# Kernel tuning notes

Measured on AMD Instinct MI355X. Metric: run time of the kernel, lower is better.

Reference implementation:

```python
import jax, jax.numpy as jnp
import numpy as np

N = 20000        # nodes
NHID = 128       # hidden channels per head
HEADS = 4
E = 320000       # edges (before self-loops)
NLAYERS = 4
NCLASS = 40
DT, ALPHA, GAMMA = 1.0, 1.0, 1.0
NEG_SLOPE = 0.2  # PyG GATConv default


def setup_inputs() -> dict:
    key = jax.random.key(0)
    ks = jax.random.split(key, 8)
    s = 1.0 / np.sqrt(NHID)
    x = jax.random.normal(ks[0], (N, NHID), jnp.float32)
    src = jax.random.randint(ks[1], (E,), 0, N, dtype=jnp.int32)
    dst = jax.random.randint(ks[2], (E,), 0, N, dtype=jnp.int32)
    W = jax.random.normal(ks[3], (NHID, HEADS * NHID), jnp.float32) * s
    att_src = jax.random.normal(ks[4], (HEADS, NHID), jnp.float32) * s
    att_dst = jax.random.normal(ks[5], (HEADS, NHID), jnp.float32) * s
    bias = jnp.zeros((HEADS * NHID,), jnp.float32)
    Wr = jax.random.normal(ks[6], (NCLASS, NHID), jnp.float32) * s
    br = jnp.zeros((NCLASS,), jnp.float32)
    return {"x": x, "src": src, "dst": dst, "W": W, "att_src": att_src,
            "att_dst": att_dst, "bias": bias, "Wr": Wr, "br": br}


def reference(x, src, dst, W, att_src, att_dst, bias, Wr, br):
    # add self loops (PyG GATConv default)
    loop = jnp.arange(N, dtype=src.dtype)
    s_idx = jnp.concatenate([src, loop])
    d_idx = jnp.concatenate([dst, loop])

    def gat(X):
        # X: [N, NHID] -> out: [N, HEADS*NHID] (head-major, as PyG concat)
        h = (X @ W).reshape(N, HEADS, NHID)                  # [N,H,C]
        a_s = jnp.einsum('nhc,hc->nh', h, att_src)            # [N,H]
        a_d = jnp.einsum('nhc,hc->nh', h, att_dst)            # [N,H]
        e = jax.nn.leaky_relu(a_s[s_idx] + a_d[d_idx], NEG_SLOPE)  # [Etot,H]
        m = jax.ops.segment_max(e, d_idx, num_segments=N)     # scatter-softmax
        ex = jnp.exp(e - m[d_idx])
        den = jax.ops.segment_sum(ex, d_idx, num_segments=N)
        alpha = ex / den[d_idx]                               # [Etot,H]
        msg = h[s_idx] * alpha[..., None]                     # [Etot,H,C]
        out = jax.ops.segment_sum(msg, d_idx, num_segments=N)  # [N,H,C]
        return out.reshape(N, HEADS * NHID) + bias

    def step(carry, _):
        X, Y = carry
        # view(N, -1, nheads).mean(-1) on head-major [N, H*C] layout
        agg = jax.nn.elu(gat(X)).reshape(N, NHID, HEADS).mean(axis=-1)
        Y2 = Y + DT * (agg - ALPHA * Y - GAMMA * X)
        X2 = X + DT * Y2
        return (X2, Y2), (X2, Y2)

    (Xf, Yf), (Xs, Ys) = jax.lax.scan(step, (x, x), None, length=NLAYERS)
    X_all = jnp.concatenate([x[:, None], jnp.moveaxis(Xs, 0, 1)], axis=1)  # [N,L+1,C]
    Y_all = jnp.concatenate([x[:, None], jnp.moveaxis(Ys, 0, 1)], axis=1)
    out = Xf @ Wr.T + br                                     # [N, NCLASS]
    return out, X_all, Y_all
```

## Files before the change

kernel.cpp:

```cpp
#include <hip/hip_runtime.h>

typedef unsigned short u16;
typedef unsigned int u32;

#define N_NODES 20000
#define NE 320000
#define NLAYERS 4
#define NCLASS 40
#define NEG_SLOPE 0.2f
#define LSTRIDE ((NLAYERS + 1) * 128)

typedef __bf16 bf16x8 __attribute__((ext_vector_type(8)));
typedef float f32x4 __attribute__((ext_vector_type(4)));

__device__ inline u16 f2bf(float f) {
    u32 u = __float_as_uint(f);
    return (u16)((u + 0x7fffu + ((u >> 16) & 1u)) >> 16);
}
__device__ inline float bf2f(u16 u) { return __uint_as_float(((u32)u) << 16); }

__global__ void k_init(const float* __restrict__ x, u16* __restrict__ Xbf,
                       float* __restrict__ Xall, float* __restrict__ Yall) {
    int t = blockIdx.x * 256 + threadIdx.x;
    if (t >= N_NODES * 128) return;
    float v = x[t];
    Xbf[t] = f2bf(v);
    int n = t >> 7, c = t & 127;
    int ob = n * LSTRIDE + c;
    Xall[ob] = v;
    Yall[ob] = v;
}

__global__ void k_trans(const float* __restrict__ W, u16* __restrict__ Wt) {
    int t = blockIdx.x * 256 + threadIdx.x;
    int k = t >> 9, col = t & 511;
    Wt[col * 128 + k] = f2bf(W[t]);
}

__global__ __launch_bounds__(256) void k_fold(const float* __restrict__ W,
                                              const float* __restrict__ att_s,
                                              const float* __restrict__ att_d,
                                              float* __restrict__ Vs, float* __restrict__ Vd) {
    int wid = (blockIdx.x * 256 + threadIdx.x) >> 6;
    int lane = threadIdx.x & 63;
    int t = wid >> 2, hd = wid & 3;
    float w0 = W[t * 512 + hd * 128 + lane];
    float w1 = W[t * 512 + hd * 128 + 64 + lane];
    float s1 = w0 * att_s[hd * 128 + lane] + w1 * att_s[hd * 128 + 64 + lane];
    float s2 = w0 * att_d[hd * 128 + lane] + w1 * att_d[hd * 128 + 64 + lane];
    for (int off = 32; off; off >>= 1) {
        s1 += __shfl_xor(s1, off);
        s2 += __shfl_xor(s2, off);
    }
    if (lane == 0) {
        Vs[t * 4 + hd] = s1;
        Vd[t * 4 + hd] = s2;
    }
}

__global__ void k_ones(int* __restrict__ counts) {
    int t = blockIdx.x * 256 + threadIdx.x;
    if (t < N_NODES) counts[t] = 1;
}
__global__ void k_count(const int* __restrict__ dst, int* __restrict__ counts) {
    int t = blockIdx.x * 256 + threadIdx.x;
    if (t < NE) atomicAdd(&counts[dst[t]], 1);
}
__global__ void k_scan(const int* __restrict__ counts, int* __restrict__ indptr,
                       int* __restrict__ cursor) {
    __shared__ int part[1024];
    int t = threadIdx.x;
    const int CH = 20;
    int c0 = t * CH;
    int s = 0;
    for (int i = 0; i < CH; i++) {
        int idx = c0 + i;
        if (idx < N_NODES) s += counts[idx];
    }
    part[t] = s;
    __syncthreads();
    for (int off = 1; off < 1024; off <<= 1) {
        int v = 0;
        if (t >= off) v = part[t - off];
        __syncthreads();
        if (t >= off) part[t] += v;
        __syncthreads();
    }
    int ex = (t == 0) ? 0 : part[t - 1];
    for (int i = 0; i < CH; i++) {
        int idx = c0 + i;
        if (idx < N_NODES) {
            indptr[idx] = ex;
            cursor[idx] = ex;
            ex += counts[idx];
        }
    }
    if (t == 1023) indptr[N_NODES] = part[1023];
}
__global__ void k_scatter(const int* __restrict__ src, const int* __restrict__ dst,
                          int* __restrict__ cursor, int* __restrict__ esrc) {
    int t = blockIdx.x * 256 + threadIdx.x;
    if (t >= NE + N_NODES) return;
    int s, d;
    if (t < NE) { s = src[t]; d = dst[t]; }
    else { s = d = t - NE; }
    int pos = atomicAdd(&cursor[d], 1);
    esrc[pos] = s;
}

__global__ __launch_bounds__(256) void k_gemm(const u16* __restrict__ Xbf,
                                              const u16* __restrict__ Wt,
                                              u16* __restrict__ hbf) {
    const int r0 = blockIdx.x * 64;
    const int c0 = blockIdx.y * 64;
    __shared__ u16 As[64 * 136];
    __shared__ u16 Bs[64 * 136];
    const int t = threadIdx.x;
    for (int i = 0; i < 4; i++) {
        int flat = i * 256 + t;
        int row = flat >> 4;
        int kc = flat & 15;
        uint4 av = make_uint4(0u, 0u, 0u, 0u);
        int gr = r0 + row;
        if (gr < N_NODES) av = *(const uint4*)(Xbf + gr * 128 + kc * 8);
        *(uint4*)(As + row * 136 + kc * 8) = av;
        uint4 bv = *(const uint4*)(Wt + (c0 + row) * 128 + kc * 8);
        *(uint4*)(Bs + row * 136 + kc * 8) = bv;
    }
    __syncthreads();
    const int wave = t >> 6, lane = t & 63;
    const int wr = (wave >> 1) * 32, wc = (wave & 1) * 32;
    const int lrow = lane & 15, quad = lane >> 4;
    f32x4 acc[2][2] = {};
    for (int kk = 0; kk < 128; kk += 32) {
        bf16x8 a[2], b[2];
        for (int mi = 0; mi < 2; mi++)
            a[mi] = *(const bf16x8*)(As + (wr + mi * 16 + lrow) * 136 + kk + quad * 8);
        for (int ni = 0; ni < 2; ni++)
            b[ni] = *(const bf16x8*)(Bs + (wc + ni * 16 + lrow) * 136 + kk + quad * 8);
        for (int mi = 0; mi < 2; mi++)
            for (int ni = 0; ni < 2; ni++)
                acc[mi][ni] = __builtin_amdgcn_mfma_f32_16x16x32_bf16(a[mi], b[ni], acc[mi][ni], 0, 0, 0);
    }
    for (int mi = 0; mi < 2; mi++)
        for (int ni = 0; ni < 2; ni++)
            for (int r = 0; r < 4; r++) {
                int row = r0 + wr + mi * 16 + quad * 4 + r;
                int col = c0 + wc + ni * 16 + lrow;
                if (row < N_NODES) hbf[row * 512 + col] = f2bf(acc[mi][ni][r]);
            }
}

__global__ __launch_bounds__(256) void k_att(const float* __restrict__ Xall, int layer,
                                             const float* __restrict__ Vs,
                                             const float* __restrict__ Vd,
                                             float* __restrict__ a_s, float* __restrict__ a_d) {
    int wid = (blockIdx.x * 256 + threadIdx.x) >> 6;
    int lane = threadIdx.x & 63;
    const float* Xr = Xall + wid * LSTRIDE + layer * 128;
    float x0 = Xr[lane], x1 = Xr[64 + lane];
    f32x4 vs0 = *(const f32x4*)(Vs + lane * 4), vs1 = *(const f32x4*)(Vs + (64 + lane) * 4);
    f32x4 vd0 = *(const f32x4*)(Vd + lane * 4), vd1 = *(const f32x4*)(Vd + (64 + lane) * 4);
    f32x4 ps = x0 * vs0 + x1 * vs1;
    f32x4 pd = x0 * vd0 + x1 * vd1;
    for (int off = 32; off; off >>= 1)
        for (int c = 0; c < 4; c++) {
            ps[c] += __shfl_xor(ps[c], off);
            pd[c] += __shfl_xor(pd[c], off);
        }
    if (lane == 0) {
        *(f32x4*)(a_s + wid * 4) = ps;
        *(f32x4*)(a_d + wid * 4) = pd;
    }
}

__global__ __launch_bounds__(256) void k_aggr(
    const int* __restrict__ indptr, const int* __restrict__ esrc,
    const float* __restrict__ a_s, const float* __restrict__ a_d,
    const u16* __restrict__ hbf, const float* __restrict__ bias,
    u16* __restrict__ Xbf, float* __restrict__ Xall, float* __restrict__ Yall,
    float* __restrict__ a_s_nxt, float* __restrict__ a_d_nxt,
    const float* __restrict__ Vs, const float* __restrict__ Vd, int layer) {
    __shared__ int s_sh[4][66];
    __shared__ alignas(16) float al_sh[4][66][4];
    int d = (blockIdx.x * 256 + threadIdx.x) >> 6;
    int lane = threadIdx.x & 63;
    int w = threadIdx.x >> 6;
    int start = indptr[d], end = indptr[d + 1];
    int deg = end - start;
    f32x4 ad = *(const f32x4*)(a_d + d * 4);
    int hd = lane >> 4;
    float acc[8] = {0.f, 0.f, 0.f, 0.f, 0.f, 0.f, 0.f, 0.f};

    auto chunk_aggr = [&](int cnt) {
        int s_cur = s_sh[w][0];
        float al_cur = al_sh[w][0][hd];
        uint4 hv = *(const uint4*)(hbf + s_cur * 512 + lane * 8);
        for (int i = 0; i < cnt; i++) {
            int s_nxt = s_sh[w][i + 1];
            float al_nxt = al_sh[w][i + 1][hd];
            uint4 hv_n = *(const uint4*)(hbf + s_nxt * 512 + lane * 8);
            u32 h0 = hv.x, h1 = hv.y, h2 = hv.z, h3 = hv.w;
            acc[0] += al_cur * __uint_as_float(h0 << 16);
            acc[1] += al_cur * __uint_as_float(h0 & 0xffff0000u);
            acc[2] += al_cur * __uint_as_float(h1 << 16);
            acc[3] += al_cur * __uint_as_float(h1 & 0xffff0000u);
            acc[4] += al_cur * __uint_as_float(h2 << 16);
            acc[5] += al_cur * __uint_as_float(h2 & 0xffff0000u);
            acc[6] += al_cur * __uint_as_float(h3 << 16);
            acc[7] += al_cur * __uint_as_float(h3 & 0xffff0000u);
            hv = hv_n;
            al_cur = al_nxt;
        }
    };

    if (deg <= 64) {
        int j = start + lane;
        int s = 0;
        f32x4 e = {-1e30f, -1e30f, -1e30f, -1e30f};
        if (j < end) {
            s = esrc[j];
            f32x4 as = *(const f32x4*)(a_s + s * 4);
            for (int c = 0; c < 4; c++) {
                float v = as[c] + ad[c];
                e[c] = v > 0.f ? v : NEG_SLOPE * v;
            }
        }
        f32x4 mx = e;
        for (int off = 32; off; off >>= 1)
            for (int c = 0; c < 4; c++) mx[c] = fmaxf(mx[c], __shfl_xor(mx[c], off));
        f32x4 p;
        for (int c = 0; c < 4; c++) p[c] = __expf(e[c] - mx[c]);
        f32x4 den = p;
        for (int off = 32; off; off >>= 1)
            for (int c = 0; c < 4; c++) den[c] += __shfl_xor(den[c], off);
        f32x4 alpha;
        for (int c = 0; c < 4; c++) alpha[c] = p[c] * (1.f / den[c]);
        s_sh[w][lane] = s;
        *(f32x4*)&al_sh[w][lane][0] = alpha;
        if (lane == 63) {
            s_sh[w][64] = 0;
            f32x4 z = {0.f, 0.f, 0.f, 0.f};
            *(f32x4*)&al_sh[w][64][0] = z;
        }
        __builtin_amdgcn_wave_barrier();
        chunk_aggr(deg);
    } else {
        f32x4 mx = {-1e30f, -1e30f, -1e30f, -1e30f};
        for (int j = start + lane; j < end; j += 64) {
            int s = esrc[j];
            f32x4 e = *(const f32x4*)(a_s + s * 4) + ad;
            for (int c = 0; c < 4; c++) {
                float v = e[c];
                v = v > 0.f ? v : NEG_SLOPE * v;
                mx[c] = fmaxf(mx[c], v);
            }
        }
        for (int off = 32; off; off >>= 1)
            for (int c = 0; c < 4; c++) mx[c] = fmaxf(mx[c], __shfl_xor(mx[c], off));
        f32x4 den = {0.f, 0.f, 0.f, 0.f};
        for (int j = start + lane; j < end; j += 64) {
            int s = esrc[j];
            f32x4 e = *(const f32x4*)(a_s + s * 4) + ad;
            for (int c = 0; c < 4; c++) {
                float v = e[c];
                v = v > 0.f ? v : NEG_SLOPE * v;
                den[c] += __expf(v - mx[c]);
            }
        }
        for (int off = 32; off; off >>= 1)
            for (int c = 0; c < 4; c++) den[c] += __shfl_xor(den[c], off);
        f32x4 rd;
        for (int c = 0; c < 4; c++) rd[c] = 1.f / den[c];
        for (int base = start; base < end; base += 64) {
            int cnt = min(64, end - base);
            int jj = base + lane;
            int s = 0;
            f32x4 alpha = {0.f, 0.f, 0.f, 0.f};
            if (jj < end) {
                s = esrc[jj];
                f32x4 e = *(const f32x4*)(a_s + s * 4) + ad;
                for (int c = 0; c < 4; c++) {
                    float v = e[c];
                    v = v > 0.f ? v : NEG_SLOPE * v;
                    alpha[c] = __expf(v - mx[c]) * rd[c];
                }
            }
            s_sh[w][lane] = s;
            *(f32x4*)&al_sh[w][lane][0] = alpha;
            if (lane == 63) {
                s_sh[w][64] = 0;
                f32x4 z = {0.f, 0.f, 0.f, 0.f};
                *(f32x4*)&al_sh[w][64][0] = z;
            }
            __builtin_amdgcn_wave_barrier();
            chunk_aggr(cnt);
            __builtin_amdgcn_wave_barrier();
        }
    }

    f32x4 b0 = *(const f32x4*)(bias + lane * 8);
    f32x4 b1 = *(const f32x4*)(bias + lane * 8 + 4);
    float g[8];
    for (int i = 0; i < 4; i++) g[i] = acc[i] + b0[i];
    for (int i = 0; i < 4; i++) g[4 + i] = acc[4 + i] + b1[i];
    for (int i = 0; i < 8; i++) {
        float v = g[i];
        g[i] = v > 0.f ? v : __expf(v) - 1.f;
    }
    float agg0 = (g[0] + g[1] + g[2] + g[3]) * 0.25f;
    float agg1 = (g[4] + g[5] + g[6] + g[7]) * 0.25f;
    int i0 = lane * 2;
    int xo = d * LSTRIDE + layer * 128 + i0;
    int no = d * LSTRIDE + (layer + 1) * 128 + i0;
    float x0 = Xall[xo], x1 = Xall[xo + 1];
    Xall[no] = agg0;
    Xall[no + 1] = agg1;
    Yall[no] = agg0 - x0;
    Yall[no + 1] = agg1 - x1;
    Xbf[d * 128 + i0] = f2bf(agg0);
    Xbf[d * 128 + i0 + 1] = f2bf(agg1);

    f32x4 vs0 = *(const f32x4*)(Vs + i0 * 4), vs1 = *(const f32x4*)(Vs + (i0 + 1) * 4);
    f32x4 vd0 = *(const f32x4*)(Vd + i0 * 4), vd1 = *(const f32x4*)(Vd + (i0 + 1) * 4);
    f32x4 ps, pd;
    for (int c = 0; c < 4; c++) {
        ps[c] = agg0 * vs0[c] + agg1 * vs1[c];
        pd[c] = agg0 * vd0[c] + agg1 * vd1[c];
    }
    for (int off = 32; off; off >>= 1)
        for (int c = 0; c < 4; c++) {
            ps[c] += __shfl_xor(ps[c], off);
            pd[c] += __shfl_xor(pd[c], off);
        }
    if (lane == 0) {
        *(f32x4*)(a_s_nxt + d * 4) = ps;
        *(f32x4*)(a_d_nxt + d * 4) = pd;
    }
}

__global__ __launch_bounds__(256) void k_out(const float* __restrict__ Xall,
                                             const float* __restrict__ Wr,
                                             const float* __restrict__ br,
                                             float* __restrict__ out) {
    __shared__ float Xs[4][128];
    int wave = threadIdx.x >> 6, lane = threadIdx.x & 63;
    int n = blockIdx.x * 4 + wave;
    const float* Xr = Xall + n * LSTRIDE + NLAYERS * 128;
    Xs[wave][lane] = Xr[lane];
    Xs[wave][64 + lane] = Xr[64 + lane];
    __syncthreads();
    if (lane < NCLASS) {
        float acc = 0.f;
        for (int kc = 0; kc < 32; kc++) {
            f32x4 wv = *(const f32x4*)(Wr + lane * 128 + kc * 4);
            for (int q = 0; q < 4; q++) acc += Xs[wave][kc * 4 + q] * wv[q];
        }
        out[n * NCLASS + lane] = acc + br[lane];
    }
}

extern "C" void kernel_launch(void* const* d_in, const int* in_sizes, int n_in,
                              void* d_out, int out_size, void* d_ws, size_t ws_size,
                              hipStream_t stream) {
    const float* x = (const float*)d_in[0];
    const int* src = (const int*)d_in[1];
    const int* dst = (const int*)d_in[2];
    const float* W = (const float*)d_in[3];
    const float* att_s = (const float*)d_in[4];
    const float* att_d = (const float*)d_in[5];
    const float* bias = (const float*)d_in[6];
    const float* Wr = (const float*)d_in[7];
    const float* br = (const float*)d_in[8];

    float* out = (float*)d_out;
    float* Xall = out + (size_t)N_NODES * NCLASS;
    float* Yall = Xall + (size_t)N_NODES * LSTRIDE;

    char* p = (char*)d_ws;
    auto alloc = [&](size_t bytes) -> char* {
        char* r = p;
        p += (bytes + 255) & ~(size_t)255;
        return r;
    };
    u16* Xbf = (u16*)alloc((size_t)N_NODES * 128 * 2);
    u16* hbf = (u16*)alloc((size_t)N_NODES * 512 * 2);
    u16* Wt = (u16*)alloc(512 * 128 * 2);
    float* a_sA = (float*)alloc((size_t)N_NODES * 4 * 4);
    float* a_dA = (float*)alloc((size_t)N_NODES * 4 * 4);
    float* a_sB = (float*)alloc((size_t)N_NODES * 4 * 4);
    float* a_dB = (float*)alloc((size_t)N_NODES * 4 * 4);
    float* Vs = (float*)alloc(128 * 4 * 4);
    float* Vd = (float*)alloc(128 * 4 * 4);
    int* indptr = (int*)alloc((N_NODES + 1) * 4);
    int* cursor = (int*)alloc(N_NODES * 4);
    int* counts = (int*)alloc(N_NODES * 4);
    int* esrc = (int*)alloc((size_t)(NE + N_NODES) * 4);

    k_init<<<(N_NODES * 128 + 255) / 256, 256, 0, stream>>>(x, Xbf, Xall, Yall);
    k_trans<<<(512 * 128) / 256, 256, 0, stream>>>(W, Wt);
    k_fold<<<128, 256, 0, stream>>>(W, att_s, att_d, Vs, Vd);
    k_ones<<<(N_NODES + 255) / 256, 256, 0, stream>>>(counts);
    k_count<<<(NE + 255) / 256, 256, 0, stream>>>(dst, counts);
    k_scan<<<1, 1024, 0, stream>>>(counts, indptr, cursor);
    k_scatter<<<(NE + N_NODES + 255) / 256, 256, 0, stream>>>(src, dst, cursor, esrc);

    k_att<<<N_NODES / 4, 256, 0, stream>>>(Xall, 0, Vs, Vd, a_sA, a_dA);

    for (int layer = 0; layer < NLAYERS; layer++) {
        const float* as_r = (layer & 1) ? a_sB : a_sA;
        const float* ad_r = (layer & 1) ? a_dB : a_dA;
        float* as_w = (layer & 1) ? a_sA : a_sB;
        float* ad_w = (layer & 1) ? a_dA : a_dB;
        k_gemm<<<dim3((N_NODES + 63) / 64, 8), 256, 0, stream>>>(Xbf, Wt, hbf);
        k_aggr<<<N_NODES / 4, 256, 0, stream>>>(indptr, esrc, as_r, ad_r, hbf, bias,
                                                Xbf, Xall, Yall, as_w, ad_w, Vs, Vd, layer);
    }
    k_out<<<N_NODES / 4, 256, 0, stream>>>(Xall, Wr, br, out);
}
```

Before: 531.3 us.

## Aggregate raw node features before projection, then apply W per head after

Uses linearity to reorder aggregate-then-project. Each layer now gathers 128-wide bf16 X rows per edge, weighted by the four head attention coefficients, instead of gathering 512-wide projected h rows. A new fused kernel multiplies the per-head aggregates by W and applies bias, ELU, head mean, state update and next-layer logits. This cuts per-edge gather traffic about fourfold and replaces the separate GEMM. The cost is a staged N×512 intermediate buffer and an extra bf16 rounding of the aggregates. It also folds the counts initialisation into k_init and skips logits on the last layer.

Measured after the change: 500.8 us. -5.8%, faster.

```diff
diff --git a/kernel.cpp b/kernel.cpp
--- a/kernel.cpp
+++ b/kernel.cpp
@@ -20,9 +20,11 @@
 __device__ inline float bf2f(u16 u) { return __uint_as_float(((u32)u) << 16); }
 
 __global__ void k_init(const float* __restrict__ x, u16* __restrict__ Xbf,
-                       float* __restrict__ Xall, float* __restrict__ Yall) {
+                       float* __restrict__ Xall, float* __restrict__ Yall,
+                       int* __restrict__ counts) {
     int t = blockIdx.x * 256 + threadIdx.x;
     if (t >= N_NODES * 128) return;
+    if (t < N_NODES) counts[t] = 1;
     float v = x[t];
     Xbf[t] = f2bf(v);
     int n = t >> 7, c = t & 127;
@@ -58,10 +60,6 @@
     }
 }
 
-__global__ void k_ones(int* __restrict__ counts) {
-    int t = blockIdx.x * 256 + threadIdx.x;
-    if (t < N_NODES) counts[t] = 1;
-}
 __global__ void k_count(const int* __restrict__ dst, int* __restrict__ counts) {
     int t = blockIdx.x * 256 + threadIdx.x;
     if (t < NE) atomicAdd(&counts[dst[t]], 1);
@@ -106,49 +104,6 @@
     else { s = d = t - NE; }
     int pos = atomicAdd(&cursor[d], 1);
     esrc[pos] = s;
-}
-
-__global__ __launch_bounds__(256) void k_gemm(const u16* __restrict__ Xbf,
-                                              const u16* __restrict__ Wt,
-                                              u16* __restrict__ hbf) {
-    const int r0 = blockIdx.x * 64;
-    const int c0 = blockIdx.y * 64;
-    __shared__ u16 As[64 * 136];
-    __shared__ u16 Bs[64 * 136];
-    const int t = threadIdx.x;
-    for (int i = 0; i < 4; i++) {
-        int flat = i * 256 + t;
-        int row = flat >> 4;
-        int kc = flat & 15;
-        uint4 av = make_uint4(0u, 0u, 0u, 0u);
-        int gr = r0 + row;
-        if (gr < N_NODES) av = *(const uint4*)(Xbf + gr * 128 + kc * 8);
-        *(uint4*)(As + row * 136 + kc * 8) = av;
-        uint4 bv = *(const uint4*)(Wt + (c0 + row) * 128 + kc * 8);
-        *(uint4*)(Bs + row * 136 + kc * 8) = bv;
-    }
-    __syncthreads();
-    const int wave = t >> 6, lane = t & 63;
-    const int wr = (wave >> 1) * 32, wc = (wave & 1) * 32;
-    const int lrow = lane & 15, quad = lane >> 4;
-    f32x4 acc[2][2] = {};
-    for (int kk = 0; kk < 128; kk += 32) {
-        bf16x8 a[2], b[2];
-        for (int mi = 0; mi < 2; mi++)
-            a[mi] = *(const bf16x8*)(As + (wr + mi * 16 + lrow) * 136 + kk + quad * 8);
-        for (int ni = 0; ni < 2; ni++)
-            b[ni] = *(const bf16x8*)(Bs + (wc + ni * 16 + lrow) * 136 + kk + quad * 8);
-        for (int mi = 0; mi < 2; mi++)
-            for (int ni = 0; ni < 2; ni++)
-                acc[mi][ni] = __builtin_amdgcn_mfma_f32_16x16x32_bf16(a[mi], b[ni], acc[mi][ni], 0, 0, 0);
-    }
-    for (int mi = 0; mi < 2; mi++)
-        for (int ni = 0; ni < 2; ni++)
-            for (int r = 0; r < 4; r++) {
-                int row = r0 + wr + mi * 16 + quad * 4 + r;
-                int col = c0 + wc + ni * 16 + lrow;
-                if (row < N_NODES) hbf[row * 512 + col] = f2bf(acc[mi][ni][r]);
-            }
 }
 
 __global__ __launch_bounds__(256) void k_att(const float* __restrict__ Xall, int layer,
@@ -177,10 +132,7 @@
 __global__ __launch_bounds__(256) void k_aggr(
     const int* __restrict__ indptr, const int* __restrict__ esrc,
     const float* __restrict__ a_s, const float* __restrict__ a_d,
-    const u16* __restrict__ hbf, const float* __restrict__ bias,
-    u16* __restrict__ Xbf, float* __restrict__ Xall, float* __restrict__ Yall,
-    float* __restrict__ a_s_nxt, float* __restrict__ a_d_nxt,
-    const float* __restrict__ Vs, const float* __restrict__ Vd, int layer) {
+    const u16* __restrict__ Xbf, u16* __restrict__ Xagg) {
     __shared__ int s_sh[4][66];
     __shared__ alignas(16) float al_sh[4][66][4];
     int d = (blockIdx.x * 256 + threadIdx.x) >> 6;
@@ -189,27 +141,22 @@
     int start = indptr[d], end = indptr[d + 1];
     int deg = end - start;
     f32x4 ad = *(const f32x4*)(a_d + d * 4);
-    int hd = lane >> 4;
-    float acc[8] = {0.f, 0.f, 0.f, 0.f, 0.f, 0.f, 0.f, 0.f};
+    f32x4 accA = {0.f, 0.f, 0.f, 0.f};
+    f32x4 accB = {0.f, 0.f, 0.f, 0.f};
 
     auto chunk_aggr = [&](int cnt) {
         int s_cur = s_sh[w][0];
-        float al_cur = al_sh[w][0][hd];
-        uint4 hv = *(const uint4*)(hbf + s_cur * 512 + lane * 8);
+        f32x4 al_cur = *(const f32x4*)&al_sh[w][0][0];
+        u32 xv = *(const u32*)(Xbf + s_cur * 128 + lane * 2);
         for (int i = 0; i < cnt; i++) {
             int s_nxt = s_sh[w][i + 1];
-            float al_nxt = al_sh[w][i + 1][hd];
-            uint4 hv_n = *(const uint4*)(hbf + s_nxt * 512 + lane * 8);
-            u32 h0 = hv.x, h1 = hv.y, h2 = hv.z, h3 = hv.w;
-            acc[0] += al_cur * __uint_as_float(h0 << 16);
-            acc[1] += al_cur * __uint_as_float(h0 & 0xffff0000u);
-            acc[2] += al_cur * __uint_as_float(h1 << 16);
-            acc[3] += al_cur * __uint_as_float(h1 & 0xffff0000u);
-            acc[4] += al_cur * __uint_as_float(h2 << 16);
-            acc[5] += al_cur * __uint_as_float(h2 & 0xffff0000u);
-            acc[6] += al_cur * __uint_as_float(h3 << 16);
-            acc[7] += al_cur * __uint_as_float(h3 & 0xffff0000u);
-            hv = hv_n;
+            f32x4 al_nxt = *(const f32x4*)&al_sh[w][i + 1][0];
+            u32 xv_n = *(const u32*)(Xbf + s_nxt * 128 + lane * 2);
+            float x0 = __uint_as_float(xv << 16);
+            float x1 = __uint_as_float(xv & 0xffff0000u);
+            accA += al_cur * x0;
+            accB += al_cur * x1;
+            xv = xv_n;
             al_cur = al_nxt;
         }
     };
@@ -299,43 +246,96 @@
         }
     }
 
-    f32x4 b0 = *(const f32x4*)(bias + lane * 8);
-    f32x4 b1 = *(const f32x4*)(bias + lane * 8 + 4);
-    float g[8];
-    for (int i = 0; i < 4; i++) g[i] = acc[i] + b0[i];
-    for (int i = 0; i < 4; i++) g[4 + i] = acc[4 + i] + b1[i];
-    for (int i = 0; i < 8; i++) {
-        float v = g[i];
-        g[i] = v > 0.f ? v : __expf(v) - 1.f;
-    }
-    float agg0 = (g[0] + g[1] + g[2] + g[3]) * 0.25f;
-    float agg1 = (g[4] + g[5] + g[6] + g[7]) * 0.25f;
-    int i0 = lane * 2;
-    int xo = d * LSTRIDE + layer * 128 + i0;
-    int no = d * LSTRIDE + (layer + 1) * 128 + i0;
-    float x0 = Xall[xo], x1 = Xall[xo + 1];
-    Xall[no] = agg0;
-    Xall[no + 1] = agg1;
-    Yall[no] = agg0 - x0;
-    Yall[no + 1] = agg1 - x1;
-    Xbf[d * 128 + i0] = f2bf(agg0);
-    Xbf[d * 128 + i0 + 1] = f2bf(agg1);
-
-    f32x4 vs0 = *(const f32x4*)(Vs + i0 * 4), vs1 = *(const f32x4*)(Vs + (i0 + 1) * 4);
-    f32x4 vd0 = *(const f32x4*)(Vd + i0 * 4), vd1 = *(const f32x4*)(Vd + (i0 + 1) * 4);
-    f32x4 ps, pd;
-    for (int c = 0; c < 4; c++) {
-        ps[c] = agg0 * vs0[c] + agg1 * vs1[c];
-        pd[c] = agg0 * vd0[c] + agg1 * vd1[c];
-    }
-    for (int off = 32; off; off >>= 1)
-        for (int c = 0; c < 4; c++) {
-            ps[c] += __shfl_xor(ps[c], off);
-            pd[c] += __shfl_xor(pd[c], off);
-        }
-    if (lane == 0) {
-        *(f32x4*)(a_s_nxt + d * 4) = ps;
-        *(f32x4*)(a_d_nxt + d * 4) = pd;
+    u16* xo = Xagg + d * 512 + lane * 2;
+    for (int hh = 0; hh < 4; hh++) {
+        u32 pk = (u32)f2bf(accA[hh]) | ((u32)f2bf(accB[hh]) << 16);
+        *(u32*)(xo + hh * 128) = pk;
+    }
+}
+
+__global__ __launch_bounds__(512) void k_fuse(
+    const u16* __restrict__ Xagg, const u16* __restrict__ Wt,
+    const float* __restrict__ bias,
+    float* __restrict__ Xall, float* __restrict__ Yall, u16* __restrict__ Xbf,
+    float* __restrict__ a_s_nxt, float* __restrict__ a_d_nxt,
+    const float* __restrict__ Vs, const float* __restrict__ Vd,
+    int layer, int do_logits) {
+    __shared__ u16 As[16 * 520];
+    __shared__ float G[16 * 528];
+    __shared__ float aggbuf[16 * 130];
+    const int t = threadIdx.x;
+    const int r0 = blockIdx.x * 16;
+    const int wv = t >> 6, lane = t & 63;
+    const int h = wv >> 1, colhalf = wv & 1;
+    const int lrow = lane & 15, quad = lane >> 4;
+
+    bf16x8 bfr[16];
+    {
+        const u16* Wb = Wt + (h * 128 + colhalf * 64) * 128;
+        for (int k4 = 0; k4 < 4; k4++)
+            for (int ni = 0; ni < 4; ni++)
+                bfr[k4 * 4 + ni] =
+                    *(const bf16x8*)(Wb + (ni * 16 + lrow) * 128 + k4 * 32 + quad * 8);
+    }
+    for (int i = 0; i < 2; i++) {
+        int flat = i * 512 + t;
+        int row = flat >> 6, kc = flat & 63;
+        *(uint4*)(As + row * 520 + kc * 8) = *(const uint4*)(Xagg + (r0 + row) * 512 + kc * 8);
+    }
+    __syncthreads();
+    f32x4 acc[4] = {};
+    for (int k4 = 0; k4 < 4; k4++) {
+        bf16x8 a = *(const bf16x8*)(As + lrow * 520 + h * 128 + k4 * 32 + quad * 8);
+        for (int ni = 0; ni < 4; ni++)
+            acc[ni] = __builtin_amdgcn_mfma_f32_16x16x32_bf16(a, bfr[k4 * 4 + ni], acc[ni], 0, 0, 0);
+    }
+    for (int ni = 0; ni < 4; ni++) {
+        int c = colhalf * 64 + ni * 16 + lrow;
+        float bv = bias[h * 128 + c];
+        for (int r = 0; r < 4; r++) {
+            float v = acc[ni][r] + bv;
+            v = v > 0.f ? v : __expf(v) - 1.f;
+            G[(quad * 4 + r) * 528 + h * 128 + c] = v;
+        }
+    }
+    __syncthreads();
+    {
+        int c = t & 127, rg = t >> 7;
+        int hh = c >> 5, cc = (c & 31) * 4;
+        for (int rr = 0; rr < 4; rr++) {
+            int row = rg * 4 + rr;
+            f32x4 gp = *(const f32x4*)&G[row * 528 + hh * 128 + cc];
+            float agg = 0.25f * (gp[0] + gp[1] + gp[2] + gp[3]);
+            aggbuf[row * 130 + c] = agg;
+            int node = r0 + row;
+            int xo = node * LSTRIDE + layer * 128 + c;
+            int no = node * LSTRIDE + (layer + 1) * 128 + c;
+            float xp = Xall[xo];
+            Xall[no] = agg;
+            Yall[no] = agg - xp;
+            Xbf[node * 128 + c] = f2bf(agg);
+        }
+    }
+    if (do_logits) {
+        __syncthreads();
+        f32x4 vs0 = *(const f32x4*)(Vs + lane * 4), vs1 = *(const f32x4*)(Vs + (64 + lane) * 4);
+        f32x4 vd0 = *(const f32x4*)(Vd + lane * 4), vd1 = *(const f32x4*)(Vd + (64 + lane) * 4);
+        for (int rr = 0; rr < 2; rr++) {
+            int row = wv * 2 + rr;
+            float x0 = aggbuf[row * 130 + lane], x1 = aggbuf[row * 130 + 64 + lane];
+            f32x4 ps = x0 * vs0 + x1 * vs1;
+            f32x4 pd = x0 * vd0 + x1 * vd1;
+            for (int off = 32; off; off >>= 1)
+                for (int c2 = 0; c2 < 4; c2++) {
+                    ps[c2] += __shfl_xor(ps[c2], off);
+                    pd[c2] += __shfl_xor(pd[c2], off);
+                }
+            if (lane == 0) {
+                int node = r0 + row;
+                *(f32x4*)(a_s_nxt + node * 4) = ps;
+                *(f32x4*)(a_d_nxt + node * 4) = pd;
+            }
+        }
     }
 }
 
@@ -384,7 +384,7 @@
         return r;
     };
     u16* Xbf = (u16*)alloc((size_t)N_NODES * 128 * 2);
-    u16* hbf = (u16*)alloc((size_t)N_NODES * 512 * 2);
+    u16* Xagg = (u16*)alloc((size_t)N_NODES * 512 * 2);
     u16* Wt = (u16*)alloc(512 * 128 * 2);
     float* a_sA = (float*)alloc((size_t)N_NODES * 4 * 4);
     float* a_dA = (float*)alloc((size_t)N_NODES * 4 * 4);
@@ -397,10 +397,9 @@
     int* counts = (int*)alloc(N_NODES * 4);
     int* esrc = (int*)alloc((size_t)(NE + N_NODES) * 4);
 
-    k_init<<<(N_NODES * 128 + 255) / 256, 256, 0, stream>>>(x, Xbf, Xall, Yall);
+    k_init<<<(N_NODES * 128 + 255) / 256, 256, 0, stream>>>(x, Xbf, Xall, Yall, counts);
     k_trans<<<(512 * 128) / 256, 256, 0, stream>>>(W, Wt);
     k_fold<<<128, 256, 0, stream>>>(W, att_s, att_d, Vs, Vd);
-    k_ones<<<(N_NODES + 255) / 256, 256, 0, stream>>>(counts);
     k_count<<<(NE + 255) / 256, 256, 0, stream>>>(dst, counts);
     k_scan<<<1, 1024, 0, stream>>>(counts, indptr, cursor);
     k_scatter<<<(NE + N_NODES + 255) / 256, 256, 0, stream>>>(src, dst, cursor, esrc);
@@ -412,9 +411,10 @@
         const float* ad_r = (layer & 1) ? a_dB : a_dA;
         float* as_w = (layer & 1) ? a_sA : a_sB;
         float* ad_w = (layer & 1) ? a_dA : a_dB;
-        k_gemm<<<dim3((N_NODES + 63) / 64, 8), 256, 0, stream>>>(Xbf, Wt, hbf);
-        k_aggr<<<N_NODES / 4, 256, 0, stream>>>(indptr, esrc, as_r, ad_r, hbf, bias,
-                                                Xbf, Xall, Yall, as_w, ad_w, Vs, Vd, layer);
+        k_aggr<<<N_NODES / 4, 256, 0, stream>>>(indptr, esrc, as_r, ad_r, Xbf, Xagg);
+        k_fuse<<<N_NODES / 16, 512, 0, stream>>>(Xagg, Wt, bias, Xall, Yall, Xbf,
+                                                 as_w, ad_w, Vs, Vd, layer,
+                                                 (layer + 1 < NLAYERS) ? 1 : 0);
     }
     k_out<<<N_NODES / 4, 256, 0, stream>>>(Xall, Wr, br, out);
 }
```
